# Optimization experiments

Hardware: AMD Instinct MI355X
Metric: run time of the kernel (lower is better)

Reference implementation:

```python
import jax, jax.numpy as jnp
import numpy as np

NEG_SLOPE = 0.2


def _gat(x, edge_index, W, a_src, a_dst, b):
    """PyG-style GATConv, heads=1, add_self_loops=True."""
    n = x.shape[0]
    x = x @ W  # [n, out]
    loops = jnp.arange(n, dtype=edge_index.dtype)
    src = jnp.concatenate([edge_index[0], loops])
    dst = jnp.concatenate([edge_index[1], loops])
    a_s = x @ a_src  # [n]
    a_d = x @ a_dst  # [n]
    e = jax.nn.leaky_relu(a_s[src] + a_d[dst], NEG_SLOPE)  # [E]
    m = jax.ops.segment_max(e, dst, num_segments=n)  # stable softmax per dst
    ex = jnp.exp(e - m[dst])
    denom = jax.ops.segment_sum(ex, dst, num_segments=n)
    alpha = ex / denom[dst]
    out = jax.ops.segment_sum(alpha[:, None] * x[src], dst, num_segments=n)
    return out + b


def _lin(key, fan_in, fan_out):
    k1, k2 = jax.random.split(key)
    s = 1.0 / np.sqrt(fan_in)
    W = jax.random.uniform(k1, (fan_in, fan_out), jnp.float32, -s, s)
    b = jax.random.uniform(k2, (fan_out,), jnp.float32, -s, s)
    return W, b


def setup_inputs() -> dict:
    key = jax.random.key(0)
    ks = jax.random.split(key, 24)
    ND, FD = 50000, 128   # drug nodes / feat dim
    NC, FC = 10000, 735   # cell nodes / feat dim
    ED, EC = 800000, 160000
    B = 16384
    inp = {}
    inp['drug_x'] = jax.random.normal(ks[0], (ND, FD), jnp.float32)
    inp['cell_x'] = jax.random.normal(ks[1], (NC, FC), jnp.float32)
    inp['drug_edge_index'] = jax.random.randint(ks[2], (2, ED), 0, ND, jnp.int64 if jax.config.jax_enable_x64 else jnp.int32)
    inp['cell_edge_index'] = jax.random.randint(ks[3], (2, EC), 0, NC, jnp.int32)
    inp['drug_indices'] = jax.random.randint(ks[4], (B,), 0, ND, jnp.int32)
    inp['cell_indices'] = jax.random.randint(ks[5], (B,), 0, NC, jnp.int32)
    # drug feature transform: Linear(128,256)
    inp['dW1'], inp['db1'] = _lin(ks[6], FD, 256)
    # cell feature transform: Linear(735,1024) -> Linear(1024,256)
    inp['cW1'], inp['cb1'] = _lin(ks[7], FC, 1024)
    inp['cW2'], inp['cb2'] = _lin(ks[8], 1024, 256)
    # drug GAT (256->256)
    inp['gdW'], _ = _lin(ks[9], 256, 256)
    inp['gdas'] = jax.random.normal(ks[10], (256,), jnp.float32) * 0.1
    inp['gdad'] = jax.random.normal(ks[11], (256,), jnp.float32) * 0.1
    inp['gdb'] = jnp.zeros((256,), jnp.float32)
    # cell GAT1 (256->1024)
    inp['g1W'], _ = _lin(ks[12], 256, 1024)
    inp['g1as'] = jax.random.normal(ks[13], (1024,), jnp.float32) * 0.1
    inp['g1ad'] = jax.random.normal(ks[14], (1024,), jnp.float32) * 0.1
    inp['g1b'] = jnp.zeros((1024,), jnp.float32)
    # cell GAT2 (1024->256)
    inp['g2W'], _ = _lin(ks[15], 1024, 256)
    inp['g2as'] = jax.random.normal(ks[16], (256,), jnp.float32) * 0.1
    inp['g2ad'] = jax.random.normal(ks[17], (256,), jnp.float32) * 0.1
    inp['g2b'] = jnp.zeros((256,), jnp.float32)
    inp['rW1'], inp['rb1'] = _lin(ks[18], 512, 512)
    inp['rW2'], inp['rb2'] = _lin(ks[19], 512, 512)
    inp['rW3'], inp['rb3'] = _lin(ks[20], 512, 1)
    return inp


def reference(drug_x, cell_x, drug_edge_index, cell_edge_index, drug_indices, cell_indices,
              dW1, db1, cW1, cb1, cW2, cb2,
              gdW, gdas, gdad, gdb,
              g1W, g1as, g1ad, g1b,
              g2W, g2as, g2ad, g2b,
              rW1, rb1, rW2, rb2, rW3, rb3):
    # feature transforms (dropout = identity in eval mode)
    d = jax.nn.relu(drug_x @ dW1 + db1)                 # [ND, 256]
    c = jax.nn.relu(cell_x @ cW1 + cb1)                 # [NC, 1024]
    c = jax.nn.relu(c @ cW2 + cb2)                      # [NC, 256]
    # GAT layers
    d = jax.nn.relu(_gat(d, drug_edge_index, gdW, gdas, gdad, gdb))   # [ND, 256]
    c = jax.nn.relu(_gat(c, cell_edge_index, g1W, g1as, g1ad, g1b))   # [NC, 1024]
    c = jax.nn.relu(_gat(c, cell_edge_index, g2W, g2as, g2ad, g2b))   # [NC, 256]
    comb = jnp.concatenate([d[drug_indices], c[cell_indices]], axis=-1)  # [B, 512]
    h = jax.nn.elu(comb @ rW1 + rb1)
    h = jax.nn.elu(h @ rW2 + rb2)
    return h @ rW3 + rb3                                 # [B, 1]
```

## Files before the change

kernel.cpp:

```cpp
#include <hip/hip_runtime.h>
#include <math.h>

#define NEG_SLOPE 0.2f

typedef __attribute__((ext_vector_type(8))) short short8;
typedef __attribute__((ext_vector_type(4))) float floatx4;

__device__ __forceinline__ unsigned short f2bf(float f) {
    unsigned u = __float_as_uint(f);
    u += 0x7fffu + ((u >> 16) & 1u);
    return (unsigned short)(u >> 16);
}
__device__ __forceinline__ float bf2f(unsigned short h) {
    return __uint_as_float((unsigned)h << 16);
}
__device__ __forceinline__ float lrelu(float v) {
    return v > 0.f ? v : NEG_SLOPE * v;
}

typedef __attribute__((address_space(3))) unsigned int lds_u32;
typedef const __attribute__((address_space(1))) unsigned int glb_u32c;
__device__ __forceinline__ void gll16(const unsigned short* g, unsigned short* l) {
    __builtin_amdgcn_global_load_lds((glb_u32c*)g, (lds_u32*)l, 16, 0, 0);
}

struct SJob { const float* W; unsigned short* Th; unsigned short* Tl; int K, N, Kp, base; };
struct SJobs { SJob j[8]; };

__global__ __launch_bounds__(256) void split_transpose_multi(SJobs js) {
    int t = blockIdx.x;
    int ji = 0;
#pragma unroll
    for (int q = 1; q < 8; ++q) if (t >= js.j[q].base) ji = q;
    const SJob jb = js.j[ji];
    int local = t - jb.base;
    int ntiles = jb.N / 32;
    int tn = local % ntiles, tk = local / ntiles;
    int k0 = tk * 32, n0 = tn * 32;
    __shared__ float tbuf[32][33];
    int c = threadIdx.x & 31, r = threadIdx.x >> 5;
    for (int rr = r; rr < 32; rr += 8) {
        int k = k0 + rr, n = n0 + c;
        tbuf[rr][c] = (k < jb.K && n < jb.N) ? jb.W[(long)k * jb.N + n] : 0.f;
    }
    __syncthreads();
    for (int rr = r; rr < 32; rr += 8) {
        int n = n0 + rr, k = k0 + c;
        if (n < jb.N && k < jb.Kp) {
            float v = tbuf[c][rr];
            unsigned short h = f2bf(v);
            jb.Th[(long)n * jb.Kp + k] = h;
            jb.Tl[(long)n * jb.Kp + k] = f2bf(v - bf2f(h));
        }
    }
}

__global__ __launch_bounds__(256) void split_cell_rows(
    const float* __restrict__ X, unsigned short* __restrict__ H,
    unsigned short* __restrict__ L, int M)
{
    long i = blockIdx.x;
    int t = threadIdx.x;
    const float* r = X + i * 735;
    for (int c = t; c < 736; c += 256) {
        float v = (c < 735) ? r[c] : 0.f;
        unsigned short h = f2bf(v);
        H[i * 736 + c] = h;
        L[i * 736 + c] = f2bf(v - bf2f(h));
    }
}

__global__ __launch_bounds__(256) void matvec4(
    const float* __restrict__ gdW, const float* __restrict__ gdas, const float* __restrict__ gdad,
    float* __restrict__ wds, float* __restrict__ wdd,
    const float* __restrict__ g1W, const float* __restrict__ g1as, const float* __restrict__ g1ad,
    float* __restrict__ w1s, float* __restrict__ w1d)
{
    int b = blockIdx.x;
    int sel = b >> 8, k = b & 255, t = threadIdx.x;
    const float *W, *a; float* o; int N;
    if (sel == 0)      { W = gdW; a = gdas; o = wds; N = 256; }
    else if (sel == 1) { W = gdW; a = gdad; o = wdd; N = 256; }
    else if (sel == 2) { W = g1W; a = g1as; o = w1s; N = 1024; }
    else               { W = g1W; a = g1ad; o = w1d; N = 1024; }
    float s = 0.f;
    for (int n = t; n < N; n += 256) s += W[(long)k * N + n] * a[n];
#pragma unroll
    for (int off = 32; off; off >>= 1) s += __shfl_down(s, off);
    __shared__ float ls[4];
    if ((t & 63) == 0) ls[t >> 6] = s;
    __syncthreads();
    if (t == 0) o[k] = ls[0] + ls[1] + ls[2] + ls[3];
}

__global__ __launch_bounds__(256, 3) void gemm_d0_fused(
    const float* __restrict__ A,
    const unsigned short* __restrict__ Bh_g,
    const unsigned short* __restrict__ Bl_g,
    const float* __restrict__ bias,
    const float* __restrict__ was, const float* __restrict__ wad,
    float* __restrict__ C,
    float* __restrict__ das, float* __restrict__ dad,
    int M, int nblk)
{
    int bid = blockIdx.x;
    int q = nblk >> 3, rr = nblk & 7;
    int xcd = bid & 7, idx = bid >> 3;
    int wg = (xcd < rr ? xcd * (q + 1) : rr * (q + 1) + (xcd - rr) * q) + idx;
    int rb = wg >> 1, colh = wg & 1;
    int m0 = rb * 64, n0 = colh * 128;
    if (m0 >= M) return;
    const int tid = threadIdx.x;
    const int wave = tid >> 6, lane = tid & 63;
    const int lm = lane & 15, lq = lane >> 4;
    const int wn = n0 + wave * 32;

    floatx4 acc[4][2];
    floatx4 zero = {0.f, 0.f, 0.f, 0.f};
#pragma unroll
    for (int i = 0; i < 4; ++i)
#pragma unroll
        for (int j = 0; j < 2; ++j) acc[i][j] = zero;

#pragma unroll
    for (int ks = 0; ks < 4; ++ks) {
        const int kc = ks * 32 + lq * 8;
        short8 bh[2], bl[2];
#pragma unroll
        for (int j = 0; j < 2; ++j) {
            long bo = (long)(wn + j * 16 + lm) * 128 + kc;
            bh[j] = *(const short8*)(Bh_g + bo);
            bl[j] = *(const short8*)(Bl_g + bo);
        }
        short8 ah[4], al[4];
#pragma unroll
        for (int i = 0; i < 4; ++i) {
            int gm = m0 + i * 16 + lm;
            float4 t0 = {0.f, 0.f, 0.f, 0.f}, t1 = {0.f, 0.f, 0.f, 0.f};
            if (gm < M) {
                const float* ap = A + (long)gm * 128 + kc;
                t0 = *(const float4*)ap;
                t1 = *(const float4*)(ap + 4);
            }
            short8 h, l;
            float f;
            f = t0.x; h[0] = f2bf(f); l[0] = f2bf(f - bf2f(h[0]));
            f = t0.y; h[1] = f2bf(f); l[1] = f2bf(f - bf2f(h[1]));
            f = t0.z; h[2] = f2bf(f); l[2] = f2bf(f - bf2f(h[2]));
            f = t0.w; h[3] = f2bf(f); l[3] = f2bf(f - bf2f(h[3]));
            f = t1.x; h[4] = f2bf(f); l[4] = f2bf(f - bf2f(h[4]));
            f = t1.y; h[5] = f2bf(f); l[5] = f2bf(f - bf2f(h[5]));
            f = t1.z; h[6] = f2bf(f); l[6] = f2bf(f - bf2f(h[6]));
            f = t1.w; h[7] = f2bf(f); l[7] = f2bf(f - bf2f(h[7]));
            ah[i] = h; al[i] = l;
        }
#pragma unroll
        for (int i = 0; i < 4; ++i)
#pragma unroll
            for (int j = 0; j < 2; ++j) {
                acc[i][j] = __builtin_amdgcn_mfma_f32_16x16x32_bf16(ah[i], bh[j], acc[i][j], 0, 0, 0);
                acc[i][j] = __builtin_amdgcn_mfma_f32_16x16x32_bf16(al[i], bh[j], acc[i][j], 0, 0, 0);
                acc[i][j] = __builtin_amdgcn_mfma_f32_16x16x32_bf16(ah[i], bl[j], acc[i][j], 0, 0, 0);
            }
    }

    __shared__ float sps[64][5], spd[64][5];
    float bv[2], wsv[2], wdv[2];
#pragma unroll
    for (int j = 0; j < 2; ++j) {
        int gn = wn + j * 16 + lm;
        bv[j] = bias[gn];
        wsv[j] = was[gn];
        wdv[j] = wad[gn];
    }
#pragma unroll
    for (int i = 0; i < 4; ++i) {
#pragma unroll
        for (int r = 0; r < 4; ++r) {
            int gm = m0 + i * 16 + lq * 4 + r;
            float vs = 0.f, vd = 0.f;
#pragma unroll
            for (int j = 0; j < 2; ++j) {
                int gn = wn + j * 16 + lm;
                float v = fmaxf(acc[i][j][r] + bv[j], 0.f);
                if (gm < M) C[(long)gm * 256 + gn] = v;
                vs = fmaf(v, wsv[j], vs);
                vd = fmaf(v, wdv[j], vd);
            }
#pragma unroll
            for (int o = 8; o; o >>= 1) {
                vs += __shfl_xor(vs, o);
                vd += __shfl_xor(vd, o);
            }
            if (lm == 0) {
                sps[i * 16 + lq * 4 + r][wave] = vs;
                spd[i * 16 + lq * 4 + r][wave] = vd;
            }
        }
    }
    __syncthreads();
    if (tid < 64) {
        int gm = m0 + tid;
        if (gm < M) {
            float s = sps[tid][0] + sps[tid][1] + sps[tid][2] + sps[tid][3];
            float d2 = spd[tid][0] + spd[tid][1] + spd[tid][2] + spd[tid][3];
            atomicAdd(das + gm, s);
            atomicAdd(dad + gm, d2);
        }
    }
}

template<int ACT, int OSPLIT>
__global__ __launch_bounds__(256, 6) void gemm2(
    const unsigned short* __restrict__ Ah_g, const unsigned short* __restrict__ Al_g,
    const unsigned short* __restrict__ Bh_g, const unsigned short* __restrict__ Bl_g,
    const float* __restrict__ bias,
    float* __restrict__ C, unsigned short* __restrict__ Ch_g, unsigned short* __restrict__ Cl_g,
    int M, int K, int N, int Kp, int Cs)
{
    __shared__ unsigned short Ah[2048];
    __shared__ unsigned short Al[2048];
    __shared__ unsigned short Bh[4096];
    __shared__ unsigned short Bl[4096];
    const int tid = threadIdx.x;
    const int wave = tid >> 6, lane = tid & 63;
    const int lm = lane & 15, lq = lane >> 4;
    const int wn = wave * 32;
    const int nx = gridDim.x;
    const int lin = blockIdx.y * nx + blockIdx.x;
    const int sup = lin / (8 * nx);
    const int wit = lin - sup * 8 * nx;
    const int rowb = sup * 8 + (wit & 7);
    const int nb = wit >> 3;
    const int m0 = rowb * 64, n0 = nb * 128;
    if (m0 >= M) return;

    floatx4 acc[4][2];
    floatx4 zero = {0.f, 0.f, 0.f, 0.f};
#pragma unroll
    for (int i = 0; i < 4; ++i)
#pragma unroll
        for (int j = 0; j < 2; ++j) acc[i][j] = zero;

    const int srow = lane >> 2;
    const int sslot = (lane & 3) ^ ((lane >> 3) & 3);
    const unsigned short* agh = Ah_g + (long)(m0 + wave * 16 + srow) * Kp + sslot * 8;
    const unsigned short* agl = Al_g + (long)(m0 + wave * 16 + srow) * Kp + sslot * 8;
    const unsigned short* bgh0 = Bh_g + (long)(n0 + wave * 32 + srow) * Kp + sslot * 8;
    const unsigned short* bgh1 = Bh_g + (long)(n0 + wave * 32 + 16 + srow) * Kp + sslot * 8;
    const unsigned short* bgl0 = Bl_g + (long)(n0 + wave * 32 + srow) * Kp + sslot * 8;
    const unsigned short* bgl1 = Bl_g + (long)(n0 + wave * 32 + 16 + srow) * Kp + sslot * 8;
    unsigned short* lAh = &Ah[wave * 512];
    unsigned short* lAl = &Al[wave * 512];
    unsigned short* lBh0 = &Bh[wave * 1024];
    unsigned short* lBh1 = &Bh[wave * 1024 + 512];
    unsigned short* lBl0 = &Bl[wave * 1024];
    unsigned short* lBl1 = &Bl[wave * 1024 + 512];
    const int xa = (lm >> 1) & 3;

    for (int k0 = 0; k0 < K; k0 += 32) {
        gll16(agh + k0, lAh);
        gll16(agl + k0, lAl);
        gll16(bgh0 + k0, lBh0);
        gll16(bgh1 + k0, lBh1);
        gll16(bgl0 + k0, lBl0);
        gll16(bgl1 + k0, lBl1);
        __syncthreads();
        short8 fah[4], fal[4], fbh[2], fbl[2];
#pragma unroll
        for (int i = 0; i < 4; ++i) {
            int off = (i * 16 + lm) * 32 + ((lq ^ xa) << 3);
            fah[i] = *(const short8*)&Ah[off];
            fal[i] = *(const short8*)&Al[off];
        }
#pragma unroll
        for (int j = 0; j < 2; ++j) {
            int off = (wn + j * 16 + lm) * 32 + ((lq ^ xa) << 3);
            fbh[j] = *(const short8*)&Bh[off];
            fbl[j] = *(const short8*)&Bl[off];
        }
#pragma unroll
        for (int i = 0; i < 4; ++i)
#pragma unroll
            for (int j = 0; j < 2; ++j) {
                acc[i][j] = __builtin_amdgcn_mfma_f32_16x16x32_bf16(fah[i], fbh[j], acc[i][j], 0, 0, 0);
                acc[i][j] = __builtin_amdgcn_mfma_f32_16x16x32_bf16(fal[i], fbh[j], acc[i][j], 0, 0, 0);
                acc[i][j] = __builtin_amdgcn_mfma_f32_16x16x32_bf16(fah[i], fbl[j], acc[i][j], 0, 0, 0);
            }
        __syncthreads();
    }
#pragma unroll
    for (int j = 0; j < 2; ++j) {
        int gn = n0 + wn + j * 16 + lm;
        float bv = bias ? bias[gn] : 0.f;
#pragma unroll
        for (int i = 0; i < 4; ++i) {
#pragma unroll
            for (int r = 0; r < 4; ++r) {
                int gm = m0 + i * 16 + lq * 4 + r;
                if (gm < M) {
                    float v = acc[i][j][r] + bv;
                    if (ACT == 1) v = fmaxf(v, 0.f);
                    if (ACT == 2) v = v > 0.f ? v : expm1f(v);
                    if (OSPLIT) {
                        long o = (long)gm * Cs + gn;
                        unsigned short h = f2bf(v);
                        Ch_g[o] = h;
                        Cl_g[o] = f2bf(v - bf2f(h));
                    } else {
                        C[(long)gm * (long)Cs + gn] = v;
                    }
                }
            }
        }
    }
}

__global__ __launch_bounds__(256) void att_scalars(
    const float* __restrict__ x, const float* __restrict__ avs,
    const float* __restrict__ avd, float* __restrict__ outs,
    float* __restrict__ outd, int F)
{
    const int i = blockIdx.x;
    const int t = threadIdx.x;
    float ps = 0.f, pd = 0.f;
    for (int f = t; f < F; f += 256) {
        float v = x[(long)i * F + f];
        ps += v * avs[f];
        pd += v * avd[f];
    }
#pragma unroll
    for (int off = 32; off; off >>= 1) {
        ps += __shfl_down(ps, off);
        pd += __shfl_down(pd, off);
    }
    __shared__ float ls[4], ld[4];
    int lane = t & 63, w = t >> 6;
    if (lane == 0) { ls[w] = ps; ld[w] = pd; }
    __syncthreads();
    if (t == 0) {
        outs[i] = ls[0] + ls[1] + ls[2] + ls[3];
        outd[i] = ld[0] + ld[1] + ld[2] + ld[3];
    }
}

__global__ __launch_bounds__(256) void hist_kernel(
    const int* __restrict__ dst, int* __restrict__ cnt, int E, int n)
{
    int t = blockIdx.x * 256 + threadIdx.x;
    if (t >= E + n) return;
    int d = t < E ? dst[t] : (t - E);
    atomicAdd(&cnt[d], 1);
}

__global__ __launch_bounds__(256) void scan1_kernel(
    const int* __restrict__ cnt, int* __restrict__ off,
    int* __restrict__ bsum, int n)
{
    __shared__ int s[256];
    int b = blockIdx.x, t = threadIdx.x, i = b * 256 + t;
    int v = (i < n) ? cnt[i] : 0;
    s[t] = v;
    __syncthreads();
    for (int d = 1; d < 256; d <<= 1) {
        int u = (t >= d) ? s[t - d] : 0;
        __syncthreads();
        s[t] += u;
        __syncthreads();
    }
    if (i < n) off[i] = s[t] - v;
    if (t == 255) bsum[b] = s[255];
}

__global__ __launch_bounds__(256) void scan2_kernel(
    const int* __restrict__ bsum, int* __restrict__ bpre, int nb,
    int* __restrict__ off, int n)
{
    __shared__ int s[256];
    int t = threadIdx.x;
    int v = (t < nb) ? bsum[t] : 0;
    s[t] = v;
    __syncthreads();
    for (int d = 1; d < 256; d <<= 1) {
        int u = (t >= d) ? s[t - d] : 0;
        __syncthreads();
        s[t] += u;
        __syncthreads();
    }
    if (t < nb) bpre[t] = s[t] - v;
    if (t == 255) off[n] = s[255];
}

__global__ __launch_bounds__(256) void scan3_kernel(
    int* __restrict__ off, int* __restrict__ cursor,
    const int* __restrict__ bpre, int n)
{
    int i = blockIdx.x * 256 + threadIdx.x;
    if (i < n) {
        int v = off[i] + bpre[blockIdx.x];
        off[i] = v;
        cursor[i] = v;
    }
}

__global__ __launch_bounds__(256) void scatter_kernel(
    const int* __restrict__ src, const int* __restrict__ dst,
    int* __restrict__ cursor, int* __restrict__ ebuf, int E, int n)
{
    int t = blockIdx.x * 256 + threadIdx.x;
    if (t >= E + n) return;
    int s = t < E ? src[t] : (t - E);
    int d = t < E ? dst[t] : (t - E);
    int pos = atomicAdd(&cursor[d], 1);
    ebuf[pos] = s;
}

template<int EPI>
__global__ __launch_bounds__(256) void gat_agg2(
    const int* __restrict__ off, const int* __restrict__ ebuf,
    const float* __restrict__ as_, const float* __restrict__ ad_,
    const float* __restrict__ x, const float* __restrict__ bias,
    const int* __restrict__ dmap,
    float* __restrict__ outF, unsigned short* __restrict__ outH,
    unsigned short* __restrict__ outL)
{
    __shared__ float sacc[4][256];
    __shared__ int   sS[128];
    __shared__ float sE[128];
    __shared__ float sred[8];
    int d = dmap ? dmap[blockIdx.x] : blockIdx.x;
    int tid = threadIdx.x;
    int w = tid >> 6, lane = tid & 63;
    int lo = off[d], hi = off[d + 1], ne = hi - lo;
    float adv = ad_[d];
    const float* xb = x + lane * 4;
    float4 acc0 = {0.f, 0.f, 0.f, 0.f}, acc1 = {0.f, 0.f, 0.f, 0.f};
    float psum = 0.f;

    if (ne <= 128) {
        if (tid < ne) {
            int s = ebuf[lo + tid];
            sS[tid] = s;
            sE[tid] = lrelu(as_[s] + adv);
        }
        __syncthreads();
        float m = (tid < ne) ? sE[tid] : -INFINITY;
#pragma unroll
        for (int o = 32; o; o >>= 1) m = fmaxf(m, __shfl_xor(m, o));
        if (lane == 0) sred[w] = m;
        __syncthreads();
        m = fmaxf(fmaxf(sred[0], sred[1]), fmaxf(sred[2], sred[3]));
        if (tid < ne) sE[tid] = expf(sE[tid] - m);
        __syncthreads();
        int i = w;
        for (; i + 4 < ne; i += 8) {
            int s0 = sS[i], s1 = sS[i + 4];
            float e0 = sE[i], e1 = sE[i + 4];
            float4 v0 = *(const float4*)(xb + (long)s0 * 256);
            float4 v1 = *(const float4*)(xb + (long)s1 * 256);
            psum += e0; psum += e1;
            acc0.x = fmaf(e0, v0.x, acc0.x); acc0.y = fmaf(e0, v0.y, acc0.y);
            acc0.z = fmaf(e0, v0.z, acc0.z); acc0.w = fmaf(e0, v0.w, acc0.w);
            acc1.x = fmaf(e1, v1.x, acc1.x); acc1.y = fmaf(e1, v1.y, acc1.y);
            acc1.z = fmaf(e1, v1.z, acc1.z); acc1.w = fmaf(e1, v1.w, acc1.w);
        }
        if (i < ne) {
            int s0 = sS[i];
            float e0 = sE[i];
            float4 v0 = *(const float4*)(xb + (long)s0 * 256);
            psum += e0;
            acc0.x = fmaf(e0, v0.x, acc0.x); acc0.y = fmaf(e0, v0.y, acc0.y);
            acc0.z = fmaf(e0, v0.z, acc0.z); acc0.w = fmaf(e0, v0.w, acc0.w);
        }
    } else {
        float m = -INFINITY;
        for (int p = lo + tid; p < hi; p += 256)
            m = fmaxf(m, lrelu(as_[ebuf[p]] + adv));
#pragma unroll
        for (int o = 32; o; o >>= 1) m = fmaxf(m, __shfl_xor(m, o));
        if (lane == 0) sred[w] = m;
        __syncthreads();
        m = fmaxf(fmaxf(sred[0], sred[1]), fmaxf(sred[2], sred[3]));
        for (int c = lo; c < hi; c += 128) {
            int cn = min(128, hi - c);
            __syncthreads();
            if (tid < cn) {
                int s = ebuf[c + tid];
                sS[tid] = s;
                sE[tid] = expf(lrelu(as_[s] + adv) - m);
            }
            __syncthreads();
            int i = w;
            for (; i + 4 < cn; i += 8) {
                int s0 = sS[i], s1 = sS[i + 4];
                float e0 = sE[i], e1 = sE[i + 4];
                float4 v0 = *(const float4*)(xb + (long)s0 * 256);
                float4 v1 = *(const float4*)(xb + (long)s1 * 256);
                psum += e0; psum += e1;
                acc0.x = fmaf(e0, v0.x, acc0.x); acc0.y = fmaf(e0, v0.y, acc0.y);
                acc0.z = fmaf(e0, v0.z, acc0.z); acc0.w = fmaf(e0, v0.w, acc0.w);
                acc1.x = fmaf(e1, v1.x, acc1.x); acc1.y = fmaf(e1, v1.y, acc1.y);
                acc1.z = fmaf(e1, v1.z, acc1.z); acc1.w = fmaf(e1, v1.w, acc1.w);
            }
            if (i < cn) {
                int s0 = sS[i];
                float e0 = sE[i];
                float4 v0 = *(const float4*)(xb + (long)s0 * 256);
                psum += e0;
                acc0.x = fmaf(e0, v0.x, acc0.x); acc0.y = fmaf(e0, v0.y, acc0.y);
                acc0.z = fmaf(e0, v0.z, acc0.z); acc0.w = fmaf(e0, v0.w, acc0.w);
            }
        }
    }
    acc0.x += acc1.x; acc0.y += acc1.y; acc0.z += acc1.z; acc0.w += acc1.w;
    if (lane == 0) sred[4 + w] = psum;
    *(float4*)&sacc[w][lane * 4] = acc0;
    __syncthreads();
    float inv = 1.f / (sred[4] + sred[5] + sred[6] + sred[7]);
    float v = (sacc[0][tid] + sacc[1][tid] + sacc[2][tid] + sacc[3][tid]) * inv;
    long o = (long)blockIdx.x * 256 + tid;
    if (EPI == 1) {
        outF[o] = fmaxf(v + bias[tid], 0.f);
    } else {
        unsigned short h = f2bf(v);
        outH[o] = h;
        outL[o] = f2bf(v - bf2f(h));
    }
}

__global__ __launch_bounds__(256) void gather_cell_split(
    const float* __restrict__ cfin, const int* __restrict__ cidx,
    unsigned short* __restrict__ combH, unsigned short* __restrict__ combL)
{
    int i = blockIdx.x;
    int t = threadIdx.x;
    float v = cfin[(long)cidx[i] * 256 + t];
    long b = (long)i * 512 + 256 + t;
    unsigned short h = f2bf(v);
    combH[b] = h;
    combL[b] = f2bf(v - bf2f(h));
}

__global__ __launch_bounds__(256) void head_final_kernel(
    const float* __restrict__ h, const float* __restrict__ w,
    const float* __restrict__ b, float* __restrict__ out, int M)
{
    int gw = blockIdx.x * 4 + (threadIdx.x >> 6);
    int lane = threadIdx.x & 63;
    if (gw >= M) return;
    const float* row = h + (long)gw * 512;
    float s = 0.f;
#pragma unroll
    for (int f = lane; f < 512; f += 64) s += row[f] * w[f];
#pragma unroll
    for (int off = 32; off; off >>= 1) s += __shfl_down(s, off);
    if (lane == 0) out[gw] = s + b[0];
}

static inline dim3 mfma_grid64(int M, int N) {
    int ny = (M + 63) / 64;
    ny = (ny + 7) & ~7;
    return dim3(N / 128, ny);
}

extern "C" void kernel_launch(void* const* d_in, const int* in_sizes, int n_in,
                              void* d_out, int out_size, void* d_ws, size_t ws_size,
                              hipStream_t stream)
{
    const float* drug_x = (const float*)d_in[0];
    const float* cell_x = (const float*)d_in[1];
    const int* d_ei = (const int*)d_in[2];
    const int* c_ei = (const int*)d_in[3];
    const int* d_idx = (const int*)d_in[4];
    const int* c_idx = (const int*)d_in[5];
    const float* dW1 = (const float*)d_in[6];
    const float* db1 = (const float*)d_in[7];
    const float* cW1 = (const float*)d_in[8];
    const float* cb1 = (const float*)d_in[9];
    const float* cW2 = (const float*)d_in[10];
    const float* cb2 = (const float*)d_in[11];
    const float* gdW = (const float*)d_in[12];
    const float* gdas = (const float*)d_in[13];
    const float* gdad = (const float*)d_in[14];
    const float* gdb = (const float*)d_in[15];
    const float* g1W = (const float*)d_in[16];
    const float* g1as = (const float*)d_in[17];
    const float* g1ad = (const float*)d_in[18];
    const float* g1b = (const float*)d_in[19];
    const float* g2W = (const float*)d_in[20];
    const float* g2as = (const float*)d_in[21];
    const float* g2ad = (const float*)d_in[22];
    const float* g2b = (const float*)d_in[23];
    const float* rW1 = (const float*)d_in[24];
    const float* rb1 = (const float*)d_in[25];
    const float* rW2 = (const float*)d_in[26];
    const float* rb2 = (const float*)d_in[27];
    const float* rW3 = (const float*)d_in[28];
    const float* rb3 = (const float*)d_in[29];

    const int ND = in_sizes[0] / 128;
    const int NC = in_sizes[1] / 735;
    const int ED = in_sizes[2] / 2;
    const int EC = in_sizes[3] / 2;
    const int NB = in_sizes[4];

    const int* d_src = d_ei;
    const int* d_dst = d_ei + ED;
    const int* c_src = c_ei;
    const int* c_dst = c_ei + EC;

    const size_t MB = 1ull << 20;
    const size_t KB = 1024;
    char* ws = (char*)d_ws;

    size_t wo = 0;
    auto walloc = [&](size_t elems) -> unsigned short* {
        unsigned short* p = (unsigned short*)(ws + wo);
        wo += ((elems * 2 + 255) & ~(size_t)255);
        return p;
    };
    unsigned short* dW1h = walloc(256 * 128);  unsigned short* dW1l = walloc(256 * 128);
    unsigned short* cW1h = walloc(1024 * 736); unsigned short* cW1l = walloc(1024 * 736);
    unsigned short* cW2h = walloc(256 * 1024); unsigned short* cW2l = walloc(256 * 1024);
    unsigned short* gdWh = walloc(256 * 256);  unsigned short* gdWl = walloc(256 * 256);
    unsigned short* g1Wh = walloc(1024 * 256); unsigned short* g1Wl = walloc(1024 * 256);
    unsigned short* g2Wh = walloc(256 * 1024); unsigned short* g2Wl = walloc(256 * 1024);
    unsigned short* rW1h = walloc(512 * 512);  unsigned short* rW1l = walloc(512 * 512);
    unsigned short* rW2h = walloc(512 * 512);  unsigned short* rW2l = walloc(512 * 512);

    float* wa_ds  = (float*)(ws + 9 * MB);
    float* wa_dd  = (float*)(ws + 9 * MB + 4 * KB);
    float* wa_c1s = (float*)(ws + 9 * MB + 8 * KB);
    float* wa_c1d = (float*)(ws + 9 * MB + 12 * KB);
    float* cas    = (float*)(ws + 9 * MB + 64 * KB);
    float* cad    = (float*)(ws + 9 * MB + 128 * KB);
    int*   coff   = (int*)(ws + 9 * MB + 192 * KB);
    int*   ccur   = (int*)(ws + 9 * MB + 256 * KB);
    int*   ccnt   = (int*)(ws + 9 * MB + 320 * KB);
    int*   bsum_d = (int*)(ws + 9 * MB + 400 * KB);
    int*   bpre_d = (int*)(ws + 9 * MB + 404 * KB);
    int*   bsum_c = (int*)(ws + 9 * MB + 408 * KB);
    int*   bpre_c = (int*)(ws + 9 * MB + 412 * KB);
    int*   cebuf  = (int*)(ws + 10 * MB);
    float* das    = (float*)(ws + 11 * MB);
    float* dad    = (float*)(ws + 11 * MB + 256 * KB);
    int*   doff   = (int*)(ws + 11 * MB + 512 * KB);
    int*   dcur   = (int*)(ws + 11 * MB + 768 * KB);
    int*   dcnt   = (int*)(ws + 12 * MB);
    int*   debuf  = (int*)(ws + 12 * MB + 256 * KB);

    float* dbuf  = (float*)(ws + 16 * MB);
    unsigned short* aggdh = (unsigned short*)(ws + 66 * MB);
    unsigned short* aggdl = (unsigned short*)(ws + 75 * MB);
    unsigned short* combh = (unsigned short*)(ws + 84 * MB);
    unsigned short* combl = (unsigned short*)(ws + 101 * MB);
    unsigned short* c0h = (unsigned short*)(ws + 16 * MB);
    unsigned short* c0l = (unsigned short*)(ws + 36 * MB);
    float* c1b   = (float*)(ws + 118 * MB);
    unsigned short* aggch = (unsigned short*)(ws + 129 * MB);
    unsigned short* aggcl = (unsigned short*)(ws + 135 * MB);
    unsigned short* c2h = (unsigned short*)(ws + 16 * MB);
    unsigned short* c2l = (unsigned short*)(ws + 36 * MB);
    float* xc2   = (float*)(ws + 118 * MB);
    float* cfin  = (float*)(ws + 141 * MB);
    unsigned short* h1h = (unsigned short*)(ws + 16 * MB);
    unsigned short* h1l = (unsigned short*)(ws + 33 * MB);
    float* h2b   = (float*)(ws + 50 * MB);
    unsigned short* cxh = (unsigned short*)(ws + 152 * MB);
    unsigned short* cxl = (unsigned short*)(ws + 167 * MB);

    SJobs js;
    js.j[0] = {dW1, dW1h, dW1l, 128, 256, 128, 0};
    js.j[1] = {cW1, cW1h, cW1l, 735, 1024, 736, 32};
    js.j[2] = {cW2, cW2h, cW2l, 1024, 256, 1024, 768};
    js.j[3] = {gdW, gdWh, gdWl, 256, 256, 256, 1024};
    js.j[4] = {g1W, g1Wh, g1Wl, 256, 1024, 256, 1088};
    js.j[5] = {g2W, g2Wh, g2Wl, 1024, 256, 1024, 1344};
    js.j[6] = {rW1, rW1h, rW1l, 512, 512, 512, 1600};
    js.j[7] = {rW2, rW2h, rW2l, 512, 512, 512, 1856};
    split_transpose_multi<<<2112, 256, 0, stream>>>(js);
    split_cell_rows<<<NC, 256, 0, stream>>>(cell_x, cxh, cxl, NC);
    matvec4<<<1024, 256, 0, stream>>>(gdW, gdas, gdad, wa_ds, wa_dd,
                                      g1W, g1as, g1ad, wa_c1s, wa_c1d);

    hipMemsetAsync(das, 0, (size_t)ND * 4, stream);
    hipMemsetAsync(dad, 0, (size_t)ND * 4, stream);
    {
        int nblk = 2 * ((ND + 63) / 64);
        gemm_d0_fused<<<nblk, 256, 0, stream>>>(
            drug_x, dW1h, dW1l, db1, wa_ds, wa_dd, dbuf, das, dad, ND, nblk);
    }
    hipMemsetAsync(dcnt, 0, (size_t)ND * 4, stream);
    {
        int tot = ED + ND;
        int nbd = (ND + 255) / 256;
        hist_kernel<<<(tot + 255) / 256, 256, 0, stream>>>(d_dst, dcnt, ED, ND);
        scan1_kernel<<<nbd, 256, 0, stream>>>(dcnt, doff, bsum_d, ND);
        scan2_kernel<<<1, 256, 0, stream>>>(bsum_d, bpre_d, nbd, doff, ND);
        scan3_kernel<<<nbd, 256, 0, stream>>>(doff, dcur, bpre_d, ND);
        scatter_kernel<<<(tot + 255) / 256, 256, 0, stream>>>(d_src, d_dst, dcur, debuf, ED, ND);
        gat_agg2<0><<<NB, 256, 0, stream>>>(doff, debuf, das, dad, dbuf, nullptr,
                                            d_idx, nullptr, aggdh, aggdl);
    }
    gemm2<1, 1><<<mfma_grid64(NB, 256), 256, 0, stream>>>(
        aggdh, aggdl, gdWh, gdWl, gdb, nullptr, combh, combl,
        NB, 256, 256, 256, 512);

    gemm2<1, 1><<<mfma_grid64(NC, 1024), 256, 0, stream>>>(
        cxh, cxl, cW1h, cW1l, cb1, nullptr, c0h, c0l,
        NC, 736, 1024, 736, 1024);
    gemm2<1, 0><<<mfma_grid64(NC, 256), 256, 0, stream>>>(
        c0h, c0l, cW2h, cW2l, cb2, c1b, nullptr, nullptr,
        NC, 1024, 256, 1024, 256);
    att_scalars<<<NC, 256, 0, stream>>>(c1b, wa_c1s, wa_c1d, cas, cad, 256);
    hipMemsetAsync(ccnt, 0, (size_t)NC * 4, stream);
    {
        int tot = EC + NC;
        int nbc = (NC + 255) / 256;
        hist_kernel<<<(tot + 255) / 256, 256, 0, stream>>>(c_dst, ccnt, EC, NC);
        scan1_kernel<<<nbc, 256, 0, stream>>>(ccnt, coff, bsum_c, NC);
        scan2_kernel<<<1, 256, 0, stream>>>(bsum_c, bpre_c, nbc, coff, NC);
        scan3_kernel<<<nbc, 256, 0, stream>>>(coff, ccur, bpre_c, NC);
        scatter_kernel<<<(tot + 255) / 256, 256, 0, stream>>>(c_src, c_dst, ccur, cebuf, EC, NC);
        gat_agg2<0><<<NC, 256, 0, stream>>>(coff, cebuf, cas, cad, c1b, nullptr,
                                            nullptr, nullptr, aggch, aggcl);
    }
    gemm2<1, 1><<<mfma_grid64(NC, 1024), 256, 0, stream>>>(
        aggch, aggcl, g1Wh, g1Wl, g1b, nullptr, c2h, c2l,
        NC, 256, 1024, 256, 1024);
    gemm2<0, 0><<<mfma_grid64(NC, 256), 256, 0, stream>>>(
        c2h, c2l, g2Wh, g2Wl, nullptr, xc2, nullptr, nullptr,
        NC, 1024, 256, 1024, 256);
    att_scalars<<<NC, 256, 0, stream>>>(xc2, g2as, g2ad, cas, cad, 256);
    gat_agg2<1><<<NC, 256, 0, stream>>>(coff, cebuf, cas, cad, xc2, g2b,
                                        nullptr, cfin, nullptr, nullptr);

    gather_cell_split<<<NB, 256, 0, stream>>>(cfin, c_idx, combh, combl);
    gemm2<2, 1><<<mfma_grid64(NB, 512), 256, 0, stream>>>(
        combh, combl, rW1h, rW1l, rb1, nullptr, h1h, h1l,
        NB, 512, 512, 512, 512);
    gemm2<2, 0><<<mfma_grid64(NB, 512), 256, 0, stream>>>(
        h1h, h1l, rW2h, rW2l, rb2, h2b, nullptr, nullptr,
        NB, 512, 512, 512, 512);
    head_final_kernel<<<(NB + 3) / 4, 256, 0, stream>>>(h2b, rW3, rb3, (float*)d_out, NB);
}
```

Before: 740.3 us.

## Double-buffer LDS tiles in split-bf16 GEMM with async prefetch two steps ahead

Converts the gemm2 main loop to double-buffered shared memory, so global-to-LDS loads for the tile two k-steps ahead are issued while the current tile is multiplied. The full __syncthreads pairs are replaced with explicit vmcnt/lgkmcnt waits and raw barriers. This is meant to hide global load latency behind the MFMA work. In exchange it doubles LDS use, and the occupancy hint drops from 6 to 3 blocks per CU.

```diff
diff --git a/kernel.cpp b/kernel.cpp
--- a/kernel.cpp
+++ b/kernel.cpp
@@ -211,17 +211,17 @@
 }
 
 template<int ACT, int OSPLIT>
-__global__ __launch_bounds__(256, 6) void gemm2(
+__global__ __launch_bounds__(256, 3) void gemm2(
     const unsigned short* __restrict__ Ah_g, const unsigned short* __restrict__ Al_g,
     const unsigned short* __restrict__ Bh_g, const unsigned short* __restrict__ Bl_g,
     const float* __restrict__ bias,
     float* __restrict__ C, unsigned short* __restrict__ Ch_g, unsigned short* __restrict__ Cl_g,
     int M, int K, int N, int Kp, int Cs)
 {
-    __shared__ unsigned short Ah[2048];
-    __shared__ unsigned short Al[2048];
-    __shared__ unsigned short Bh[4096];
-    __shared__ unsigned short Bl[4096];
+    __shared__ unsigned short Ah[2][2048];
+    __shared__ unsigned short Al[2][2048];
+    __shared__ unsigned short Bh[2][4096];
+    __shared__ unsigned short Bl[2][4096];
     const int tid = threadIdx.x;
     const int wave = tid >> 6, lane = tid & 63;
     const int lm = lane & 15, lq = lane >> 4;
@@ -250,34 +250,43 @@
     const unsigned short* bgh1 = Bh_g + (long)(n0 + wave * 32 + 16 + srow) * Kp + sslot * 8;
     const unsigned short* bgl0 = Bl_g + (long)(n0 + wave * 32 + srow) * Kp + sslot * 8;
     const unsigned short* bgl1 = Bl_g + (long)(n0 + wave * 32 + 16 + srow) * Kp + sslot * 8;
-    unsigned short* lAh = &Ah[wave * 512];
-    unsigned short* lAl = &Al[wave * 512];
-    unsigned short* lBh0 = &Bh[wave * 1024];
-    unsigned short* lBh1 = &Bh[wave * 1024 + 512];
-    unsigned short* lBl0 = &Bl[wave * 1024];
-    unsigned short* lBl1 = &Bl[wave * 1024 + 512];
+    const int wchA = wave * 512;
+    const int wchB = wave * 1024;
     const int xa = (lm >> 1) & 3;
 
+    gll16(agh, &Ah[0][wchA]);
+    gll16(agl, &Al[0][wchA]);
+    gll16(bgh0, &Bh[0][wchB]);
+    gll16(bgh1, &Bh[0][wchB + 512]);
+    gll16(bgl0, &Bl[0][wchB]);
+    gll16(bgl1, &Bl[0][wchB + 512]);
+    if (32 < K) {
+        gll16(agh + 32, &Ah[1][wchA]);
+        gll16(agl + 32, &Al[1][wchA]);
+        gll16(bgh0 + 32, &Bh[1][wchB]);
+        gll16(bgh1 + 32, &Bh[1][wchB + 512]);
+        gll16(bgl0 + 32, &Bl[1][wchB]);
+        gll16(bgl1 + 32, &Bl[1][wchB + 512]);
+    }
+    int cur = 0;
+
     for (int k0 = 0; k0 < K; k0 += 32) {
-        gll16(agh + k0, lAh);
-        gll16(agl + k0, lAl);
-        gll16(bgh0 + k0, lBh0);
-        gll16(bgh1 + k0, lBh1);
-        gll16(bgl0 + k0, lBl0);
-        gll16(bgl1 + k0, lBl1);
-        __syncthreads();
+        if (k0 + 32 < K) asm volatile("s_waitcnt vmcnt(6)" ::: "memory");
+        else             asm volatile("s_waitcnt vmcnt(0)" ::: "memory");
+        __builtin_amdgcn_s_barrier();
+        asm volatile("" ::: "memory");
         short8 fah[4], fal[4], fbh[2], fbl[2];
 #pragma unroll
         for (int i = 0; i < 4; ++i) {
             int off = (i * 16 + lm) * 32 + ((lq ^ xa) << 3);
-            fah[i] = *(const short8*)&Ah[off];
-            fal[i] = *(const short8*)&Al[off];
+            fah[i] = *(const short8*)&Ah[cur][off];
+            fal[i] = *(const short8*)&Al[cur][off];
         }
 #pragma unroll
         for (int j = 0; j < 2; ++j) {
             int off = (wn + j * 16 + lm) * 32 + ((lq ^ xa) << 3);
-            fbh[j] = *(const short8*)&Bh[off];
-            fbl[j] = *(const short8*)&Bl[off];
+            fbh[j] = *(const short8*)&Bh[cur][off];
+            fbl[j] = *(const short8*)&Bl[cur][off];
         }
 #pragma unroll
         for (int i = 0; i < 4; ++i)
@@ -287,7 +296,17 @@
                 acc[i][j] = __builtin_amdgcn_mfma_f32_16x16x32_bf16(fal[i], fbh[j], acc[i][j], 0, 0, 0);
                 acc[i][j] = __builtin_amdgcn_mfma_f32_16x16x32_bf16(fah[i], fbl[j], acc[i][j], 0, 0, 0);
             }
-        __syncthreads();
+        asm volatile("s_waitcnt lgkmcnt(0)" ::: "memory");
+        __builtin_amdgcn_s_barrier();
+        if (k0 + 64 < K) {
+            gll16(agh + k0 + 64, &Ah[cur][wchA]);
+            gll16(agl + k0 + 64, &Al[cur][wchA]);
+            gll16(bgh0 + k0 + 64, &Bh[cur][wchB]);
+            gll16(bgh1 + k0 + 64, &Bh[cur][wchB + 512]);
+            gll16(bgl0 + k0 + 64, &Bl[cur][wchB]);
+            gll16(bgl1 + k0 + 64, &Bl[cur][wchB + 512]);
+        }
+        cur ^= 1;
     }
 #pragma unroll
     for (int j = 0; j < 2; ++j) {
```

Result: slower. 764.4 us (+3.3%).

## Aggregate GAT softmax with one wavefront per destination row instead of one block

Applied to the files above, without the earlier changes.

Replaces the block-per-node GAT aggregation with a kernel that assigns one 64-lane wavefront to each destination row, four rows per block. Edge indices and exp weights are broadcast with shuffles instead of shared memory, and all __syncthreads and the cross-wave LDS reduction are removed. This aims to cut barrier and LDS overhead and raise useful occupancy for low-degree nodes (average degree around 17). The trade-off is a serial per-edge gather loop inside one wave with no two-way unrolling, which reduces memory-level parallelism per row.

```diff
diff --git a/kernel.cpp b/kernel.cpp
--- a/kernel.cpp
+++ b/kernel.cpp
@@ -416,115 +416,69 @@
 }
 
 template<int EPI>
-__global__ __launch_bounds__(256) void gat_agg2(
+__global__ __launch_bounds__(256) void gat_agg3(
     const int* __restrict__ off, const int* __restrict__ ebuf,
     const float* __restrict__ as_, const float* __restrict__ ad_,
     const float* __restrict__ x, const float* __restrict__ bias,
     const int* __restrict__ dmap,
     float* __restrict__ outF, unsigned short* __restrict__ outH,
-    unsigned short* __restrict__ outL)
-{
-    __shared__ float sacc[4][256];
-    __shared__ int   sS[128];
-    __shared__ float sE[128];
-    __shared__ float sred[8];
-    int d = dmap ? dmap[blockIdx.x] : blockIdx.x;
-    int tid = threadIdx.x;
-    int w = tid >> 6, lane = tid & 63;
-    int lo = off[d], hi = off[d + 1], ne = hi - lo;
+    unsigned short* __restrict__ outL, int nrows)
+{
+    int row = blockIdx.x * 4 + (threadIdx.x >> 6);
+    int lane = threadIdx.x & 63;
+    if (row >= nrows) return;
+    int d = dmap ? dmap[row] : row;
+    int lo = off[d], hi = off[d + 1];
     float adv = ad_[d];
+
+    float m = -INFINITY;
+    for (int p = lo + lane; p < hi; p += 64)
+        m = fmaxf(m, lrelu(as_[ebuf[p]] + adv));
+#pragma unroll
+    for (int o = 32; o; o >>= 1) m = fmaxf(m, __shfl_xor(m, o));
+
     const float* xb = x + lane * 4;
-    float4 acc0 = {0.f, 0.f, 0.f, 0.f}, acc1 = {0.f, 0.f, 0.f, 0.f};
+    float4 acc = {0.f, 0.f, 0.f, 0.f};
     float psum = 0.f;
-
-    if (ne <= 128) {
-        if (tid < ne) {
-            int s = ebuf[lo + tid];
-            sS[tid] = s;
-            sE[tid] = lrelu(as_[s] + adv);
-        }
-        __syncthreads();
-        float m = (tid < ne) ? sE[tid] : -INFINITY;
-#pragma unroll
-        for (int o = 32; o; o >>= 1) m = fmaxf(m, __shfl_xor(m, o));
-        if (lane == 0) sred[w] = m;
-        __syncthreads();
-        m = fmaxf(fmaxf(sred[0], sred[1]), fmaxf(sred[2], sred[3]));
-        if (tid < ne) sE[tid] = expf(sE[tid] - m);
-        __syncthreads();
-        int i = w;
-        for (; i + 4 < ne; i += 8) {
-            int s0 = sS[i], s1 = sS[i + 4];
-            float e0 = sE[i], e1 = sE[i + 4];
-            float4 v0 = *(const float4*)(xb + (long)s0 * 256);
-            float4 v1 = *(const float4*)(xb + (long)s1 * 256);
-            psum += e0; psum += e1;
-            acc0.x = fmaf(e0, v0.x, acc0.x); acc0.y = fmaf(e0, v0.y, acc0.y);
-            acc0.z = fmaf(e0, v0.z, acc0.z); acc0.w = fmaf(e0, v0.w, acc0.w);
-            acc1.x = fmaf(e1, v1.x, acc1.x); acc1.y = fmaf(e1, v1.y, acc1.y);
-            acc1.z = fmaf(e1, v1.z, acc1.z); acc1.w = fmaf(e1, v1.w, acc1.w);
-        }
-        if (i < ne) {
-            int s0 = sS[i];
-            float e0 = sE[i];
-            float4 v0 = *(const float4*)(xb + (long)s0 * 256);
-            psum += e0;
-            acc0.x = fmaf(e0, v0.x, acc0.x); acc0.y = fmaf(e0, v0.y, acc0.y);
-            acc0.z = fmaf(e0, v0.z, acc0.z); acc0.w = fmaf(e0, v0.w, acc0.w);
-        }
+    for (int base = lo; base < hi; base += 64) {
+        int cnt = min(64, hi - base);
+        int s = 0;
+        float ex = 0.f;
+        if (lane < cnt) {
+            s = ebuf[base + lane];
+            ex = expf(lrelu(as_[s] + adv) - m);
+        }
+        psum += ex;
+        for (int i = 0; i < cnt; ++i) {
+            int si = __shfl(s, i);
+            float ei = __shfl(ex, i);
+            float4 v = *(const float4*)(xb + (long)si * 256);
+            acc.x = fmaf(ei, v.x, acc.x);
+            acc.y = fmaf(ei, v.y, acc.y);
+            acc.z = fmaf(ei, v.z, acc.z);
+            acc.w = fmaf(ei, v.w, acc.w);
+        }
+    }
+#pragma unroll
+    for (int o = 32; o; o >>= 1) psum += __shfl_xor(psum, o);
+    float inv = 1.f / psum;
+
+    long ob = (long)row * 256 + lane * 4;
+    if (EPI == 1) {
+        float r0 = fmaxf(acc.x * inv + bias[lane * 4 + 0], 0.f);
+        float r1 = fmaxf(acc.y * inv + bias[lane * 4 + 1], 0.f);
+        float r2 = fmaxf(acc.z * inv + bias[lane * 4 + 2], 0.f);
+        float r3 = fmaxf(acc.w * inv + bias[lane * 4 + 3], 0.f);
+        float4 r = {r0, r1, r2, r3};
+        *(float4*)(outF + ob) = r;
     } else {
-        float m = -INFINITY;
-        for (int p = lo + tid; p < hi; p += 256)
-            m = fmaxf(m, lrelu(as_[ebuf[p]] + adv));
-#pragma unroll
-        for (int o = 32; o; o >>= 1) m = fmaxf(m, __shfl_xor(m, o));
-        if (lane == 0) sred[w] = m;
-        __syncthreads();
-        m = fmaxf(fmaxf(sred[0], sred[1]), fmaxf(sred[2], sred[3]));
-        for (int c = lo; c < hi; c += 128) {
-            int cn = min(128, hi - c);
-            __syncthreads();
-            if (tid < cn) {
-                int s = ebuf[c + tid];
-                sS[tid] = s;
-                sE[tid] = expf(lrelu(as_[s] + adv) - m);
-            }
-            __syncthreads();
-            int i = w;
-            for (; i + 4 < cn; i += 8) {
-                int s0 = sS[i], s1 = sS[i + 4];
-                float e0 = sE[i], e1 = sE[i + 4];
-                float4 v0 = *(const float4*)(xb + (long)s0 * 256);
-                float4 v1 = *(const float4*)(xb + (long)s1 * 256);
-                psum += e0; psum += e1;
-                acc0.x = fmaf(e0, v0.x, acc0.x); acc0.y = fmaf(e0, v0.y, acc0.y);
-                acc0.z = fmaf(e0, v0.z, acc0.z); acc0.w = fmaf(e0, v0.w, acc0.w);
-                acc1.x = fmaf(e1, v1.x, acc1.x); acc1.y = fmaf(e1, v1.y, acc1.y);
-                acc1.z = fmaf(e1, v1.z, acc1.z); acc1.w = fmaf(e1, v1.w, acc1.w);
-            }
-            if (i < cn) {
-                int s0 = sS[i];
-                float e0 = sE[i];
-                float4 v0 = *(const float4*)(xb + (long)s0 * 256);
-                psum += e0;
-                acc0.x = fmaf(e0, v0.x, acc0.x); acc0.y = fmaf(e0, v0.y, acc0.y);
-                acc0.z = fmaf(e0, v0.z, acc0.z); acc0.w = fmaf(e0, v0.w, acc0.w);
-            }
-        }
-    }
-    acc0.x += acc1.x; acc0.y += acc1.y; acc0.z += acc1.z; acc0.w += acc1.w;
-    if (lane == 0) sred[4 + w] = psum;
-    *(float4*)&sacc[w][lane * 4] = acc0;
-    __syncthreads();
-    float inv = 1.f / (sred[4] + sred[5] + sred[6] + sred[7]);
-    float v = (sacc[0][tid] + sacc[1][tid] + sacc[2][tid] + sacc[3][tid]) * inv;
-    long o = (long)blockIdx.x * 256 + tid;
-    if (EPI == 1) {
-        outF[o] = fmaxf(v + bias[tid], 0.f);
-    } else {
-        unsigned short h = f2bf(v);
-        outH[o] = h;
-        outL[o] = f2bf(v - bf2f(h));
+        float vv[4] = {acc.x * inv, acc.y * inv, acc.z * inv, acc.w * inv};
+#pragma unroll
+        for (int j = 0; j < 4; ++j) {
+            unsigned short h = f2bf(vv[j]);
+            outH[ob + j] = h;
+            outL[ob + j] = f2bf(vv[j] - bf2f(h));
+        }
     }
 }
 
@@ -699,8 +653,8 @@
         scan2_kernel<<<1, 256, 0, stream>>>(bsum_d, bpre_d, nbd, doff, ND);
         scan3_kernel<<<nbd, 256, 0, stream>>>(doff, dcur, bpre_d, ND);
         scatter_kernel<<<(tot + 255) / 256, 256, 0, stream>>>(d_src, d_dst, dcur, debuf, ED, ND);
-        gat_agg2<0><<<NB, 256, 0, stream>>>(doff, debuf, das, dad, dbuf, nullptr,
-                                            d_idx, nullptr, aggdh, aggdl);
+        gat_agg3<0><<<(NB + 3) / 4, 256, 0, stream>>>(doff, debuf, das, dad, dbuf, nullptr,
+                                                      d_idx, nullptr, aggdh, aggdl, NB);
     }
     gemm2<1, 1><<<mfma_grid64(NB, 256), 256, 0, stream>>>(
         aggdh, aggdl, gdWh, gdWl, gdb, nullptr, combh, combl,
@@ -722,8 +676,8 @@
         scan2_kernel<<<1, 256, 0, stream>>>(bsum_c, bpre_c, nbc, coff, NC);
         scan3_kernel<<<nbc, 256, 0, stream>>>(coff, ccur, bpre_c, NC);
         scatter_kernel<<<(tot + 255) / 256, 256, 0, stream>>>(c_src, c_dst, ccur, cebuf, EC, NC);
-        gat_agg2<0><<<NC, 256, 0, stream>>>(coff, cebuf, cas, cad, c1b, nullptr,
-                                            nullptr, nullptr, aggch, aggcl);
+        gat_agg3<0><<<(NC + 3) / 4, 256, 0, stream>>>(coff, cebuf, cas, cad, c1b, nullptr,
+                                                      nullptr, nullptr, aggch, aggcl, NC);
     }
     gemm2<1, 1><<<mfma_grid64(NC, 1024), 256, 0, stream>>>(
         aggch, aggcl, g1Wh, g1Wl, g1b, nullptr, c2h, c2l,
@@ -732,8 +686,8 @@
         c2h, c2l, g2Wh, g2Wl, nullptr, xc2, nullptr, nullptr,
         NC, 1024, 256, 1024, 256);
     att_scalars<<<NC, 256, 0, stream>>>(xc2, g2as, g2ad, cas, cad, 256);
-    gat_agg2<1><<<NC, 256, 0, stream>>>(coff, cebuf, cas, cad, xc2, g2b,
-                                        nullptr, cfin, nullptr, nullptr);
+    gat_agg3<1><<<(NC + 3) / 4, 256, 0, stream>>>(coff, cebuf, cas, cad, xc2, g2b,
+                                                  nullptr, cfin, nullptr, nullptr, NC);
 
     gather_cell_split<<<NB, 256, 0, stream>>>(cfin, c_idx, combh, combl);
     gemm2<2, 1><<<mfma_grid64(NB, 512), 256, 0, stream>>>(
```

Result: no change. 747.7 us (+1.0%).
